# Kernel tuning notes

Hardware: AMD Instinct MI355X
Metric: run time of the kernel (lower is better)

## Reference

```python
import jax, jax.numpy as jnp
import numpy as np

THETA = 0.7
KS = 3          # deformable-conv kernel size
N = KS * KS     # 9 sampling points


def setup_inputs() -> dict:
    key = jax.random.key(0)
    k = jax.random.split(key, 7)
    B, C, H, W = 2, 256, 64, 64
    x = jax.random.normal(k[0], (B, C, H, W), jnp.float32)
    # offset-predicting conv (3x3, pad 1), 2*N output channels; small init so offsets are sane
    p_w = jax.random.normal(k[1], (2 * N, C, 3, 3), jnp.float32) * 0.01
    p_b = jax.random.normal(k[2], (2 * N,), jnp.float32) * 0.01
    # modulation conv (3x3, pad 1), N output channels
    m_w = jax.random.normal(k[3], (N, C, 3, 3), jnp.float32) * 0.01
    m_b = jnp.zeros((N,), jnp.float32)
    # final deform conv weight (applied as ks x ks, stride ks over the unfolded map), no bias
    dconv_w = jax.random.normal(k[4], (256, C, KS, KS), jnp.float32) * 0.05
    # central-difference conv raw weight, shape (Cout, Cin, 1, 5), no bias
    cdc_w = jax.random.normal(k[5], (256, C, 1, 5), jnp.float32) * 0.05
    return {"x": x, "p_w": p_w, "p_b": p_b, "m_w": m_w, "m_b": m_b,
            "dconv_w": dconv_w, "cdc_w": cdc_w}


def _conv2d(x, w, pad):
    return jax.lax.conv_general_dilated(
        x, w, window_strides=(1, 1), padding=pad,
        dimension_numbers=("NCHW", "OIHW", "NCHW"))


def deform_conv(x, p_w, p_b, m_w, m_b, dconv_w):
    B, C, H, W = x.shape
    same = [(1, 1), (1, 1)]
    offset = _conv2d(x, p_w, same) + p_b[None, :, None, None]          # [B,2N,H,W]
    m = jax.nn.sigmoid(_conv2d(x, m_w, same) + m_b[None, :, None, None])  # [B,N,H,W]

    xp = jnp.pad(x, ((0, 0), (0, 0), (1, 1), (1, 1)))  # zero padding 1
    Hp, Wp = H + 2, W + 2

    # p = p_0 + p_n + offset  (x = row coord, y = col coord; torch meshgrid 'ij')
    p_n_x = jnp.repeat(jnp.arange(-1, 2, dtype=x.dtype), 3)   # [-1,-1,-1,0,0,0,1,1,1]
    p_n_y = jnp.tile(jnp.arange(-1, 2, dtype=x.dtype), 3)     # [-1,0,1,-1,0,1,-1,0,1]
    rows = jnp.arange(1, H + 1, dtype=x.dtype)                # p_0_x
    cols = jnp.arange(1, W + 1, dtype=x.dtype)                # p_0_y
    px = offset[:, :N] + p_n_x[None, :, None, None] + rows[None, None, :, None]
    py = offset[:, N:] + p_n_y[None, :, None, None] + cols[None, None, None, :]
    px = jnp.transpose(px, (0, 2, 3, 1))  # [B,H,W,N]
    py = jnp.transpose(py, (0, 2, 3, 1))

    # integer corners from UNCLAMPED p (detached), as in the original
    fx = jnp.floor(jax.lax.stop_gradient(px))
    fy = jnp.floor(jax.lax.stop_gradient(py))
    qx0 = jnp.clip(fx, 0, Hp - 1)
    qy0 = jnp.clip(fy, 0, Wp - 1)
    qx1 = jnp.clip(fx + 1, 0, Hp - 1)
    qy1 = jnp.clip(fy + 1, 0, Wp - 1)

    # clamp p before computing bilinear weights (original order)
    pxc = jnp.clip(px, 0, Hp - 1)
    pyc = jnp.clip(py, 0, Wp - 1)
    g_lt = (1 + (qx0 - pxc)) * (1 + (qy0 - pyc))
    g_rb = (1 - (qx1 - pxc)) * (1 - (qy1 - pyc))
    g_lb = (1 + (qx0 - pxc)) * (1 - (qy1 - pyc))
    g_rt = (1 - (qx1 - pxc)) * (1 + (qy0 - pyc))

    xf = xp.reshape(B, C, Hp * Wp)

    def gather(qx, qy):
        idx = (qx.astype(jnp.int32) * Wp + qy.astype(jnp.int32)).reshape(B, 1, -1)
        return jnp.take_along_axis(xf, idx, axis=2).reshape(B, C, H, W, N)

    x_off = (g_lt[:, None] * gather(qx0, qy0)
             + g_rb[:, None] * gather(qx1, qy1)
             + g_lb[:, None] * gather(qx0, qy1)
             + g_rt[:, None] * gather(qx1, qy0))          # [B,C,H,W,N]
    x_off = x_off * jnp.transpose(m, (0, 2, 3, 1))[:, None]  # modulation broadcast over C

    # conv(ksxks, stride ks) over the unfolded map == contraction over the N taps;
    # tap n = 3r + c corresponds to kernel position (r, c)
    w = dconv_w.reshape(dconv_w.shape[0], C, N)
    return jnp.einsum("bchwn,ocn->bohw", x_off, w)


def cdc_conv(x, cdc_w):
    Co, Ci = cdc_w.shape[0], cdc_w.shape[1]
    z = jnp.zeros((Co, Ci, 1), cdc_w.dtype)
    wk = jnp.concatenate(
        [z, cdc_w[:, :, :, 0], z, cdc_w[:, :, :, 1], cdc_w[:, :, :, 2],
         cdc_w[:, :, :, 3], z, cdc_w[:, :, :, 4], z], axis=2
    ).reshape(Co, Ci, 3, 3)
    out_normal = _conv2d(x, wk, [(1, 1), (1, 1)])
    kdiff = cdc_w.sum(axis=(2, 3))[:, :, None, None]
    out_diff = _conv2d(x, kdiff, [(0, 0), (0, 0)])
    return out_normal - THETA * out_diff


def reference(x, p_w, p_b, m_w, m_b, dconv_w, cdc_w):
    out_dc = jax.nn.relu(deform_conv(x, p_w, p_b, m_w, m_b, dconv_w))
    out_cdc = jax.nn.relu(cdc_conv(x, cdc_w))
    return jnp.concatenate([out_dc, out_cdc], axis=1)  # [B,512,H,W]
```

## Files before the change

### kernel.cpp

```cpp
#include <hip/hip_runtime.h>
#include <hip/hip_bf16.h>
#include <math.h>

#define XT_BSTRIDE (66*66*256)
#define THETA_ 0.7f

typedef unsigned short u16;
typedef __attribute__((ext_vector_type(8))) short bf16x8;
typedef __attribute__((ext_vector_type(4))) float f32x4;

#define GLOAD16(gp, lp) __builtin_amdgcn_global_load_lds( \
    (const __attribute__((address_space(1))) unsigned int*)(gp), \
    (__attribute__((address_space(3))) unsigned int*)(lp), 16, 0, 0)

__device__ __forceinline__ float bf2f(u16 v) {
  union { unsigned u; float f; } x; x.u = ((unsigned)v) << 16; return x.f;
}
__device__ __forceinline__ u16 f2bf(float f) {
  __hip_bfloat16 h = __float2bfloat16(f);
  return *(u16*)&h;
}

__device__ __forceinline__ size_t swz_idx(int row, int k, int KT) {
  int kt = k >> 6, kc = (k >> 3) & 7, kj = k & 7;
  return (size_t)row * KT + kt * 64 + ((kc ^ (row & 7)) << 3) + kj;
}

__global__ __launch_bounds__(256) void prep(
    const float* __restrict__ x, const float* __restrict__ p_w,
    const float* __restrict__ m_w, const float* __restrict__ dconv_w,
    const float* __restrict__ cdc_w, u16* __restrict__ xTb,
    u16* __restrict__ W1t, u16* __restrict__ Wdt, u16* __restrict__ Wct) {
  int blk = blockIdx.x;
  if (blk < 512) {
    int cg = blk & 3;
    int h  = (blk >> 2) & 63;
    int b  = blk >> 8;
    __shared__ float tile[64][65];
    const float* xp = x + ((size_t)(b * 256 + cg * 64)) * 4096 + h * 64;
#pragma unroll
    for (int j = 0; j < 16; j++) {
      int idx = j * 256 + threadIdx.x;
      int ci = idx >> 6, w = idx & 63;
      tile[ci][w] = xp[(size_t)ci * 4096 + w];
    }
    __syncthreads();
    u16* xo = xTb + (size_t)b * XT_BSTRIDE + ((h + 1) * 66 + 1) * 256 + cg * 64;
#pragma unroll
    for (int j = 0; j < 16; j++) {
      int idx = j * 256 + threadIdx.x;
      int w = idx >> 6, ci = idx & 63;
      xo[(size_t)w * 256 + ci] = f2bf(tile[ci][w]);
    }
    return;
  }
  if (blk < 1032) {
    int i = (blk - 512) * 256 + threadIdx.x;
    if (i >= 133120) return;
    int c = i & 255;
    int j = i >> 8;
    int b = (j >= 260) ? 1 : 0;
    int r = j - b * 260;
    int hp, wp;
    if (r < 66)       { hp = 0;        wp = r; }
    else if (r < 132) { hp = 65;       wp = r - 66; }
    else if (r < 196) { hp = r - 131;  wp = 0; }
    else              { hp = r - 195;  wp = 65; }
    xTb[(size_t)b * XT_BSTRIDE + (hp * 66 + wp) * 256 + c] = 0;
    return;
  }
  int i = (blk - 1032) * 256 + threadIdx.x;
  if (i < 73728) {
    int o = i / 2304, k = i % 2304;
    int kp = k >> 8, c = k & 255;
    float v = 0.f;
    if (o < 18)      v = p_w[((size_t)o * 256 + c) * 9 + kp];
    else if (o < 27) v = m_w[((size_t)(o - 18) * 256 + c) * 9 + kp];
    W1t[swz_idx(o, k, 2304)] = f2bf(v);
    return;
  }
  int j = i - 73728;
  if (j < 589824) {
    int o = j / 2304, k = j % 2304;
    int n = k >> 8, c = k & 255;
    Wdt[swz_idx(o, k, 2304)] = f2bf(dconv_w[((size_t)o * 256 + c) * 9 + n]);
    return;
  }
  int j2 = j - 589824;
  if (j2 < 327680) {
    int o = j2 / 1280, k = j2 % 1280;
    int t = k >> 8, c = k & 255;
    const float* cw = cdc_w + ((size_t)o * 256 + c) * 5;
    float v = cw[t];
    if (t == 2) v -= THETA_ * (cw[0] + cw[1] + cw[2] + cw[3] + cw[4]);
    Wct[swz_idx(o, k, 1280)] = f2bf(v);
  }
}

__global__ __launch_bounds__(256) void sample_params(
    const float* __restrict__ omp, const float* __restrict__ p_b,
    const float* __restrict__ m_b, int4* __restrict__ sidx,
    float4* __restrict__ sg) {
  int i = blockIdx.x * 256 + threadIdx.x;
  if (i >= 73728) return;
  int n = i % 9;
  int p = i / 9;
  int b = p >> 12;
  int hw = p & 4095;
  int h = hw >> 6, w = hw & 63;
  float offx = p_b[n], offy = p_b[9 + n], mraw = m_b[n];
#pragma unroll
  for (int ks = 0; ks < 4; ks++) {
    const float* base = omp + ks * 221184 + b * 110592;
    offx += base[(size_t)n * 4096 + hw];
    offy += base[(size_t)(9 + n) * 4096 + hw];
    mraw += base[(size_t)(18 + n) * 4096 + hw];
  }
  float px = offx + (float)(h + n / 3);
  float py = offy + (float)(w + n % 3);
  float fx = floorf(px), fy = floorf(py);
  float qx0 = fminf(fmaxf(fx, 0.f), 65.f);
  float qy0 = fminf(fmaxf(fy, 0.f), 65.f);
  float qx1 = fminf(fmaxf(fx + 1.f, 0.f), 65.f);
  float qy1 = fminf(fmaxf(fy + 1.f, 0.f), 65.f);
  float pxc = fminf(fmaxf(px, 0.f), 65.f);
  float pyc = fminf(fmaxf(py, 0.f), 65.f);
  float gx0 = 1.f + (qx0 - pxc);
  float gx1 = 1.f - (qx1 - pxc);
  float gy0 = 1.f + (qy0 - pyc);
  float gy1 = 1.f - (qy1 - pyc);
  float m = 1.f / (1.f + expf(-mraw));
  sidx[i] = make_int4((int)qx0 * 66 + (int)qy0, (int)qx1 * 66 + (int)qy1,
                      (int)qx0 * 66 + (int)qy1, (int)qx1 * 66 + (int)qy0);
  sg[i] = make_float4(gx0 * gy0 * m, gx1 * gy1 * m, gx0 * gy1 * m, gx1 * gy0 * m);
}

__device__ __forceinline__ void offmod_body(
    const u16* __restrict__ xTb, const u16* __restrict__ Bt,
    float* __restrict__ outp, int mt, int kt0, int nkt, u16* As, u16* Bs) {
  int tid = threadIdx.x;
  int wid = tid >> 6, lane = tid & 63;
  int pbase = mt * 128;
  int l8 = lane >> 3, l7 = lane & 7;
  int lr = lane & 15, lg = lane >> 4;

  f32x4 acc[2][2];
#pragma unroll
  for (int i = 0; i < 2; i++)
#pragma unroll
    for (int j = 0; j < 2; j++) acc[i][j] = {0.f, 0.f, 0.f, 0.f};

  auto stage = [&](int kt, u16* Ah, u16* Bh) {
    int t = kt >> 2, c0 = (kt & 3) << 6;
    int dh = t / 3, dw = t % 3;
#pragma unroll
    for (int i = 0; i < 4; i++) {
      int r0 = wid * 32 + i * 8;
      int r = r0 + l8;
      int p = pbase + r;
      int b = p >> 12, hw = p & 4095, h = hw >> 6, w = hw & 63;
      int chunk = l7 ^ (r & 7);
      const u16* g = xTb + (size_t)b * XT_BSTRIDE +
                     ((h + dh) * 66 + (w + dw)) * 256 + c0 + (chunk << 3);
      GLOAD16(g, &Ah[r0 * 64]);
    }
    {
      int o0 = wid * 8;
      const u16* g = Bt + (size_t)(o0 + l8) * 2304 + kt * 64 + (l7 << 3);
      GLOAD16(g, &Bh[o0 * 64]);
    }
  };

  stage(kt0, As, Bs);
  __syncthreads();

  for (int it = 0; it < nkt; it++) {
    int cur = it & 1;
    u16* Ac = As + cur * (128 * 64);
    u16* Bc = Bs + cur * (32 * 64);
    if (it + 1 < nkt)
      stage(kt0 + it + 1, As + (cur ^ 1) * (128 * 64), Bs + (cur ^ 1) * (32 * 64));

    bf16x8 av[2][2], bv[2][2];
#pragma unroll
    for (int mf = 0; mf < 2; mf++) {
      int r = wid * 32 + mf * 16 + lr;
#pragma unroll
      for (int ks = 0; ks < 2; ks++) {
        int kc = ks * 4 + lg;
        av[mf][ks] = *(const bf16x8*)&Ac[r * 64 + ((kc ^ (r & 7)) << 3)];
      }
    }
#pragma unroll
    for (int nf = 0; nf < 2; nf++) {
      int o = nf * 16 + lr;
#pragma unroll
      for (int ks = 0; ks < 2; ks++) {
        int kc = ks * 4 + lg;
        bv[nf][ks] = *(const bf16x8*)&Bc[o * 64 + ((kc ^ (o & 7)) << 3)];
      }
    }
#pragma unroll
    for (int nf = 0; nf < 2; nf++)
#pragma unroll
      for (int mf = 0; mf < 2; mf++)
#pragma unroll
        for (int ks = 0; ks < 2; ks++)
          acc[nf][mf] = __builtin_amdgcn_mfma_f32_16x16x32_bf16(
              bv[nf][ks], av[mf][ks], acc[nf][mf], 0, 0, 0);
    __syncthreads();
  }

#pragma unroll
  for (int nf = 0; nf < 2; nf++)
#pragma unroll
    for (int mf = 0; mf < 2; mf++) {
      int p = pbase + wid * 32 + mf * 16 + lr;
      int hw = p & 4095, b = p >> 12;
      int o0 = nf * 16 + lg * 4;
      f32x4 v = acc[nf][mf];
#pragma unroll
      for (int e = 0; e < 4; e++) {
        int o = o0 + e;
        if (o < 27)
          outp[(size_t)(b * 27 + o) * 4096 + hw] = v[e];
      }
    }
}

__global__ __launch_bounds__(256) void gemm_offmod(const u16* __restrict__ xTb,
                                                   const u16* __restrict__ W1t,
                                                   float* __restrict__ omp) {
  __shared__ u16 As[2 * 128 * 64];
  __shared__ u16 Bs[2 * 32 * 64];
  int bid = blockIdx.x;
  int xcd = bid & 7;
  int i = bid >> 3;
  int mt = xcd * 8 + (i & 7);
  int ks = i >> 3;
  offmod_body(xTb, W1t, omp + ks * 221184, mt, ks * 9, 9, As, Bs);
}

__device__ void deform_body(const u16* __restrict__ xTb,
                            const u16* __restrict__ Wdt,
                            const int4* __restrict__ sidx,
                            const float4* __restrict__ sg,
                            float* __restrict__ out, int mt, u16* S) {
  const int NKT = 36;
  int tid = threadIdx.x;
  int wid = tid >> 6, lane = tid & 63;
  int l8 = lane >> 3, l7 = lane & 7;
  int lr = lane & 15, lg = lane >> 4;
  int pbase = mt * 32;
  int b = pbase >> 12;
  const u16* xb = xTb + (size_t)b * XT_BSTRIDE;

  int gr = tid >> 3;
  int gp = pbase + gr;
  int kc = tid & 7;

  f32x4 acc[4][2];
#pragma unroll
  for (int i = 0; i < 4; i++)
#pragma unroll
    for (int j = 0; j < 2; j++) acc[i][j] = {0.f, 0.f, 0.f, 0.f};

  u16* A0 = S;
  u16* B0 = S + 4096;

  int4 qi = sidx[gp * 9 + 0];
  float4 g = sg[gp * 9 + 0];
  int4 qi_n = sidx[gp * 9 + 1];
  float4 g_n = sg[gp * 9 + 1];

  bf16x8 c0r, c1r, c2r, c3r;
  float4 gc;
  bf16x8 br[8];

  auto issueA = [&](int kt) {
    int c0 = (kt & 3) << 6;
    const u16* xc = xb + c0 + (kc << 3);
    c0r = *(const bf16x8*)(xc + (size_t)qi.x * 256);
    c1r = *(const bf16x8*)(xc + (size_t)qi.y * 256);
    c2r = *(const bf16x8*)(xc + (size_t)qi.z * 256);
    c3r = *(const bf16x8*)(xc + (size_t)qi.w * 256);
    gc = g;
  };
  auto issueB = [&](int kt) {
#pragma unroll
    for (int i = 0; i < 8; i++) {
      int o0 = wid * 64 + i * 8;
      br[i] = *(const bf16x8*)(Wdt + (size_t)(o0 + l8) * 2304 + kt * 64 + (l7 << 3));
    }
  };
  auto writeA = [&](u16* Ah) {
    bf16x8 p;
#pragma unroll
    for (int j = 0; j < 8; j++) {
      float v = gc.x * bf2f((u16)c0r[j]) + gc.y * bf2f((u16)c1r[j]) +
                gc.z * bf2f((u16)c2r[j]) + gc.w * bf2f((u16)c3r[j]);
      p[j] = (short)f2bf(v);
    }
    *(bf16x8*)&Ah[gr * 64 + ((kc ^ (gr & 7)) << 3)] = p;
  };
  auto writeB = [&](u16* Bh) {
#pragma unroll
    for (int i = 0; i < 8; i++) {
      int o0 = wid * 64 + i * 8;
      *(bf16x8*)&Bh[(o0 + l8) * 64 + (l7 << 3)] = br[i];
    }
  };

  issueA(0);
  issueB(0);
  writeA(A0);
  writeB(B0);
  __syncthreads();

  for (int it = 0; it < NKT; it++) {
    int cur = it & 1;
    u16* Ac = A0 + cur * 2048;
    u16* Bc = B0 + cur * 16384;

    if (it + 1 < NKT) {
      if (((it + 1) & 3) == 0) {
        qi = qi_n; g = g_n;
        int tapn = ((it + 1) >> 2) + 1;
        if (tapn < 9) { qi_n = sidx[gp * 9 + tapn]; g_n = sg[gp * 9 + tapn]; }
      }
      issueA(it + 1);
      issueB(it + 1);
    }

    bf16x8 av[2][2], bv[4][2];
#pragma unroll
    for (int mf = 0; mf < 2; mf++) {
      int r = mf * 16 + lr;
#pragma unroll
      for (int ks = 0; ks < 2; ks++) {
        int kk = ks * 4 + lg;
        av[mf][ks] = *(const bf16x8*)&Ac[r * 64 + ((kk ^ (r & 7)) << 3)];
      }
    }
#pragma unroll
    for (int nf = 0; nf < 4; nf++) {
      int o = wid * 64 + nf * 16 + lr;
#pragma unroll
      for (int ks = 0; ks < 2; ks++) {
        int kk = ks * 4 + lg;
        bv[nf][ks] = *(const bf16x8*)&Bc[o * 64 + ((kk ^ (o & 7)) << 3)];
      }
    }
    __builtin_amdgcn_s_setprio(1);
#pragma unroll
    for (int nf = 0; nf < 4; nf++)
#pragma unroll
      for (int mf = 0; mf < 2; mf++)
#pragma unroll
        for (int ks = 0; ks < 2; ks++)
          acc[nf][mf] = __builtin_amdgcn_mfma_f32_16x16x32_bf16(
              bv[nf][ks], av[mf][ks], acc[nf][mf], 0, 0, 0);
    __builtin_amdgcn_s_setprio(0);
    __builtin_amdgcn_sched_barrier(0);

    if (it + 1 < NKT) {
      writeA(A0 + (cur ^ 1) * 2048);
      writeB(B0 + (cur ^ 1) * 16384);
    }
    __syncthreads();
  }

#pragma unroll
  for (int nf = 0; nf < 4; nf++)
#pragma unroll
    for (int mf = 0; mf < 2; mf++) {
      int p = pbase + mf * 16 + lr;
      int hw = p & 4095;
      int og = wid * 64 + nf * 16 + lg * 4;
      f32x4 v = acc[nf][mf];
#pragma unroll
      for (int e = 0; e < 4; e++)
        out[(size_t)(b * 512 + og + e) * 4096 + hw] = fmaxf(v[e], 0.f);
    }
}

__device__ void cdc_body(const u16* __restrict__ xTb,
                         const u16* __restrict__ Wct,
                         float* __restrict__ out, int mt, int nt, u16* S) {
  const int NKT = 20;
  int tid = threadIdx.x;
  int wid = tid >> 6, lane = tid & 63;
  int wr = wid >> 1, wc = wid & 1;
  int l8 = lane >> 3, l7 = lane & 7;
  int lr = lane & 15, lg = lane >> 4;
  int pbase = mt * 64;
  int obase = nt * 64;
  int b = pbase >> 12;

  f32x4 acc[2][2];
#pragma unroll
  for (int i = 0; i < 2; i++)
#pragma unroll
    for (int j = 0; j < 2; j++) acc[i][j] = {0.f, 0.f, 0.f, 0.f};

  const int dh1[5] = {0, 1, 1, 1, 2}, dw1[5] = {1, 0, 1, 2, 1};
  u16* A0 = S;
  u16* B0 = S + 8192;

  auto stage = [&](int kt, u16* Ah, u16* Bh) {
    int t = kt >> 2, c0 = (kt & 3) << 6;
    int dh = dh1[t], dw = dw1[t];
#pragma unroll
    for (int i = 0; i < 2; i++) {
      int r0 = wid * 16 + i * 8;
      int r = r0 + l8;
      int p = pbase + r;
      int hw = p & 4095, h = hw >> 6, w = hw & 63;
      int chunk = l7 ^ (r & 7);
      const u16* g = xTb + (size_t)b * XT_BSTRIDE +
                     ((h + dh) * 66 + (w + dw)) * 256 + c0 + (chunk << 3);
      GLOAD16(g, &Ah[r0 * 64]);
    }
#pragma unroll
    for (int i = 0; i < 2; i++) {
      int o0 = wid * 16 + i * 8;
      const u16* g = Wct + (size_t)(obase + o0 + l8) * 1280 + kt * 64 + (l7 << 3);
      GLOAD16(g, &Bh[o0 * 64]);
    }
  };

  stage(0, A0, B0);
  __syncthreads();

  for (int it = 0; it < NKT; it++) {
    int cur = it & 1;
    u16* Ac = A0 + cur * 4096;
    u16* Bc = B0 + cur * 4096;
    if (it + 1 < NKT)
      stage(it + 1, A0 + (cur ^ 1) * 4096, B0 + (cur ^ 1) * 4096);

    bf16x8 av[2][2], bv[2][2];
#pragma unroll
    for (int mf = 0; mf < 2; mf++) {
      int r = wr * 32 + mf * 16 + lr;
#pragma unroll
      for (int ks = 0; ks < 2; ks++) {
        int kk = ks * 4 + lg;
        av[mf][ks] = *(const bf16x8*)&Ac[r * 64 + ((kk ^ (r & 7)) << 3)];
      }
    }
#pragma unroll
    for (int nf = 0; nf < 2; nf++) {
      int o = wc * 32 + nf * 16 + lr;
#pragma unroll
      for (int ks = 0; ks < 2; ks++) {
        int kk = ks * 4 + lg;
        bv[nf][ks] = *(const bf16x8*)&Bc[o * 64 + ((kk ^ (o & 7)) << 3)];
      }
    }
#pragma unroll
    for (int nf = 0; nf < 2; nf++)
#pragma unroll
      for (int mf = 0; mf < 2; mf++)
#pragma unroll
        for (int ks = 0; ks < 2; ks++)
          acc[nf][mf] = __builtin_amdgcn_mfma_f32_16x16x32_bf16(
              bv[nf][ks], av[mf][ks], acc[nf][mf], 0, 0, 0);
    __syncthreads();
  }

#pragma unroll
  for (int nf = 0; nf < 2; nf++)
#pragma unroll
    for (int mf = 0; mf < 2; mf++) {
      int p = pbase + wr * 32 + mf * 16 + lr;
      int hw = p & 4095;
      int og = 256 + obase + wc * 32 + nf * 16 + lg * 4;
      f32x4 v = acc[nf][mf];
#pragma unroll
      for (int e = 0; e < 4; e++)
        out[(size_t)(b * 512 + og + e) * 4096 + hw] = fmaxf(v[e], 0.f);
    }
}

__global__ __launch_bounds__(256, 2) void gemm_main(
    const u16* __restrict__ xTb, const u16* __restrict__ Wdt,
    const u16* __restrict__ Wct, const int4* __restrict__ sidx,
    const float4* __restrict__ sg, float* __restrict__ out) {
  __shared__ u16 S[36864];
  int bid = blockIdx.x;
  if (bid < 256) {
    int mt = (bid & 7) * 32 + (bid >> 3);
    deform_body(xTb, Wdt, sidx, sg, out, mt, S);
  } else {
    int i = bid - 256;
    int xcd = i & 7;
    int j = i >> 3;
    int mt = xcd * 16 + (j & 15);
    int nt = j >> 4;
    cdc_body(xTb, Wct, out, mt, nt, S);
  }
}

extern "C" void kernel_launch(void* const* d_in, const int* in_sizes, int n_in,
                              void* d_out, int out_size, void* d_ws, size_t ws_size,
                              hipStream_t stream) {
  (void)in_sizes; (void)n_in; (void)out_size; (void)ws_size;
  const float* x       = (const float*)d_in[0];
  const float* p_w     = (const float*)d_in[1];
  const float* p_b     = (const float*)d_in[2];
  const float* m_w     = (const float*)d_in[3];
  const float* m_b     = (const float*)d_in[4];
  const float* dconv_w = (const float*)d_in[5];
  const float* cdc_w   = (const float*)d_in[6];
  float* out = (float*)d_out;
  char* ws = (char*)d_ws;

  u16*   xTb  = (u16*)(ws);
  float* omp  = (float*)(ws + 4460544);
  u16*   W1t  = (u16*)(ws + 7999488);
  u16*   Wdt  = (u16*)(ws + 8146944);
  u16*   Wct  = (u16*)(ws + 9326592);
  int4*  sidx = (int4*)(ws + 9981952);
  float4* sg  = (float4*)(ws + 11161600);

  prep<<<4904, 256, 0, stream>>>(x, p_w, m_w, dconv_w, cdc_w, xTb, W1t, Wdt, Wct);
  gemm_offmod<<<256, 256, 0, stream>>>(xTb, W1t, omp);
  sample_params<<<288, 256, 0, stream>>>(omp, p_b, m_b, sidx, sg);
  gemm_main<<<768, 256, 0, stream>>>(xTb, Wdt, Wct, sidx, sg, out);
}
```

Baseline: 63.24 us.

## Split deform GEMM over output channels, shrink LDS, and interleave block families

The deform GEMM tile is split in half along output channels (128 per block instead of 256), which halves accumulators, B registers and the LDS buffer so four blocks can fit per CU. The grid grows to 1024 blocks, and deform and CDC blocks are interleaved by parity with XCD-aware tile mapping to balance the two workloads. The s_setprio and sched_barrier hints are removed. In exchange, the bilinear gather and interpolation of the A tile is now done twice per pixel tile, once in each of the two output-channel halves.

```diff
diff --git a/kernel.cpp b/kernel.cpp
--- a/kernel.cpp
+++ b/kernel.cpp
@@ -245,23 +245,22 @@
                             const u16* __restrict__ Wdt,
                             const int4* __restrict__ sidx,
                             const float4* __restrict__ sg,
-                            float* __restrict__ out, int mt, u16* S) {
+                            float* __restrict__ out, int mt, int nt, u16* S) {
   const int NKT = 36;
   int tid = threadIdx.x;
   int wid = tid >> 6, lane = tid & 63;
-  int l8 = lane >> 3, l7 = lane & 7;
   int lr = lane & 15, lg = lane >> 4;
   int pbase = mt * 32;
+  int obase = nt * 128;
   int b = pbase >> 12;
   const u16* xb = xTb + (size_t)b * XT_BSTRIDE;
 
   int gr = tid >> 3;
   int gp = pbase + gr;
   int kc = tid & 7;
-
-  f32x4 acc[4][2];
-#pragma unroll
-  for (int i = 0; i < 4; i++)
+  f32x4 acc[2][2];
+#pragma unroll
+  for (int i = 0; i < 2; i++)
 #pragma unroll
     for (int j = 0; j < 2; j++) acc[i][j] = {0.f, 0.f, 0.f, 0.f};
 
@@ -275,7 +274,7 @@
 
   bf16x8 c0r, c1r, c2r, c3r;
   float4 gc;
-  bf16x8 br[8];
+  bf16x8 br[4];
 
   auto issueA = [&](int kt) {
     int c0 = (kt & 3) << 6;
@@ -288,9 +287,10 @@
   };
   auto issueB = [&](int kt) {
 #pragma unroll
-    for (int i = 0; i < 8; i++) {
-      int o0 = wid * 64 + i * 8;
-      br[i] = *(const bf16x8*)(Wdt + (size_t)(o0 + l8) * 2304 + kt * 64 + (l7 << 3));
+    for (int i = 0; i < 4; i++) {
+      int cid = i * 256 + tid;
+      int row = cid >> 3, kch = cid & 7;
+      br[i] = *(const bf16x8*)(Wdt + (size_t)(obase + row) * 2304 + kt * 64 + (kch << 3));
     }
   };
   auto writeA = [&](u16* Ah) {
@@ -305,9 +305,10 @@
   };
   auto writeB = [&](u16* Bh) {
 #pragma unroll
-    for (int i = 0; i < 8; i++) {
-      int o0 = wid * 64 + i * 8;
-      *(bf16x8*)&Bh[(o0 + l8) * 64 + (l7 << 3)] = br[i];
+    for (int i = 0; i < 4; i++) {
+      int cid = i * 256 + tid;
+      int row = cid >> 3, kch = cid & 7;
+      *(bf16x8*)&Bh[row * 64 + (kch << 3)] = br[i];
     }
   };
 
@@ -320,7 +321,7 @@
   for (int it = 0; it < NKT; it++) {
     int cur = it & 1;
     u16* Ac = A0 + cur * 2048;
-    u16* Bc = B0 + cur * 16384;
+    u16* Bc = B0 + cur * 8192;
 
     if (it + 1 < NKT) {
       if (((it + 1) & 3) == 0) {
@@ -332,7 +333,7 @@
       issueB(it + 1);
     }
 
-    bf16x8 av[2][2], bv[4][2];
+    bf16x8 av[2][2], bv[2][2];
 #pragma unroll
     for (int mf = 0; mf < 2; mf++) {
       int r = mf * 16 + lr;
@@ -343,40 +344,37 @@
       }
     }
 #pragma unroll
-    for (int nf = 0; nf < 4; nf++) {
-      int o = wid * 64 + nf * 16 + lr;
+    for (int nf = 0; nf < 2; nf++) {
+      int o = wid * 32 + nf * 16 + lr;
 #pragma unroll
       for (int ks = 0; ks < 2; ks++) {
         int kk = ks * 4 + lg;
         bv[nf][ks] = *(const bf16x8*)&Bc[o * 64 + ((kk ^ (o & 7)) << 3)];
       }
     }
-    __builtin_amdgcn_s_setprio(1);
-#pragma unroll
-    for (int nf = 0; nf < 4; nf++)
+#pragma unroll
+    for (int nf = 0; nf < 2; nf++)
 #pragma unroll
       for (int mf = 0; mf < 2; mf++)
 #pragma unroll
         for (int ks = 0; ks < 2; ks++)
           acc[nf][mf] = __builtin_amdgcn_mfma_f32_16x16x32_bf16(
               bv[nf][ks], av[mf][ks], acc[nf][mf], 0, 0, 0);
-    __builtin_amdgcn_s_setprio(0);
-    __builtin_amdgcn_sched_barrier(0);
 
     if (it + 1 < NKT) {
       writeA(A0 + (cur ^ 1) * 2048);
-      writeB(B0 + (cur ^ 1) * 16384);
+      writeB(B0 + (cur ^ 1) * 8192);
     }
     __syncthreads();
   }
 
 #pragma unroll
-  for (int nf = 0; nf < 4; nf++)
+  for (int nf = 0; nf < 2; nf++)
 #pragma unroll
     for (int mf = 0; mf < 2; mf++) {
       int p = pbase + mf * 16 + lr;
       int hw = p & 4095;
-      int og = wid * 64 + nf * 16 + lg * 4;
+      int og = obase + wid * 32 + nf * 16 + lg * 4;
       f32x4 v = acc[nf][mf];
 #pragma unroll
       for (int e = 0; e < 4; e++)
@@ -483,19 +481,21 @@
     }
 }
 
-__global__ __launch_bounds__(256, 2) void gemm_main(
+__global__ __launch_bounds__(256, 4) void gemm_main(
     const u16* __restrict__ xTb, const u16* __restrict__ Wdt,
     const u16* __restrict__ Wct, const int4* __restrict__ sidx,
     const float4* __restrict__ sg, float* __restrict__ out) {
-  __shared__ u16 S[36864];
+  __shared__ u16 S[20480];
   int bid = blockIdx.x;
-  if (bid < 256) {
-    int mt = (bid & 7) * 32 + (bid >> 3);
-    deform_body(xTb, Wdt, sidx, sg, out, mt, S);
+  int fam = bid & 1;
+  int idx = bid >> 1;
+  int xcd = idx & 7;
+  int j = idx >> 3;
+  if (fam == 0) {
+    int mt = xcd * 32 + (j & 31);
+    int nt = j >> 5;
+    deform_body(xTb, Wdt, sidx, sg, out, mt, nt, S);
   } else {
-    int i = bid - 256;
-    int xcd = i & 7;
-    int j = i >> 3;
     int mt = xcd * 16 + (j & 15);
     int nt = j >> 4;
     cdc_body(xTb, Wct, out, mt, nt, S);
@@ -527,5 +527,5 @@
   prep<<<4904, 256, 0, stream>>>(x, p_w, m_w, dconv_w, cdc_w, xTb, W1t, Wdt, Wct);
   gemm_offmod<<<256, 256, 0, stream>>>(xTb, W1t, omp);
   sample_params<<<288, 256, 0, stream>>>(omp, p_b, m_b, sidx, sg);
-  gemm_main<<<768, 256, 0, stream>>>(xTb, Wdt, Wct, sidx, sg, out);
-}
+  gemm_main<<<1024, 256, 0, stream>>>(xTb, Wdt, Wct, sidx, sg, out);
+}
```

Measured after the change: 73.26 us. +15.8%, slower.
